# Kernel optimization log

Hardware: AMD Instinct MI355X
Metric: run time of the kernel (lower is better)

Reference implementation:

```python
import jax, jax.numpy as jnp
import numpy as np

EPS = 1e-5

def setup_inputs() -> dict:
    key = jax.random.key(0)
    k1, k2, k3 = jax.random.split(key, 3)
    B, C, V, L, O = 16, 64, 20000, 9, 64
    x = jax.random.normal(k1, (B, C, V), dtype=jnp.float32)
    spiral_idx = jax.random.randint(k2, (V, L), 0, V, dtype=jnp.int32)
    W = jax.random.normal(k3, (O, C * L), dtype=jnp.float32) * 0.02
    b = jnp.zeros((O,), dtype=jnp.float32)
    gamma = jnp.ones((O,), dtype=jnp.float32)
    beta = jnp.zeros((O,), dtype=jnp.float32)
    return {"x": x, "spiral_idx": spiral_idx, "W": W, "b": b, "gamma": gamma, "beta": beta}

def reference(x, spiral_idx, W, b, gamma, beta):
    B, C, V = x.shape
    L = spiral_idx.shape[1]
    # spiral neighbor gather: neigh[b,c,v,l] = x[b,c,spiral_idx[v,l]]  -> [B,C,V,L]
    neigh = x[:, :, spiral_idx]
    # faithful row-major reshape as in the torch module (mixes V and L)
    neigh = neigh.reshape(B, C * L, V)
    # 1x1 Conv1d == matmul over channel dim
    out = jnp.einsum('om,bmv->bov', W, neigh) + b[None, :, None]
    # BatchNorm1d (training mode: biased batch stats over B and V)
    mean = out.mean(axis=(0, 2), keepdims=True)
    var = ((out - mean) ** 2).mean(axis=(0, 2), keepdims=True)
    y = gamma[None, :, None] * (out - mean) * jax.lax.rsqrt(var + EPS) + beta[None, :, None]
    return jnp.maximum(y, 0.0)
```

## Files before the change

### kernel.cpp

```cpp
#include <hip/hip_runtime.h>
#include <hip/hip_bf16.h>
#include <cstdint>
#include <cstddef>

#define B_ 16
#define C_ 64
#define V_ 20000
#define L_ 9
#define O_ 64
#define K_ 576
#define NBV (B_*V_)
#define TPB 79
#define NB1 (TPB*8)
#define NBLK (TPB*16)

typedef short bf16x8 __attribute__((ext_vector_type(8)));
typedef float f32x4  __attribute__((ext_vector_type(4)));

__device__ inline unsigned short f2bf(float f) {
    union { float f; unsigned u; } x; x.f = f;
    unsigned r = (x.u + 0x7fffu + ((x.u >> 16) & 1u)) >> 16;
    return (unsigned short)r;
}

__global__ __launch_bounds__(256) void k_tx(const float* __restrict__ x,
                                            ushort* __restrict__ xTb) {
    __shared__ float t[C_][33];
    const int b  = blockIdx.y;
    const int v0 = blockIdx.x * 32;
    const int tid = threadIdx.x;
    {
        const int c  = tid >> 2;
        const int jj = tid & 3;
        const float* src = x + ((size_t)b * C_ + c) * V_ + v0 + jj * 8;
        float4 f0 = ((const float4*)src)[0];
        float4 f1 = ((const float4*)src)[1];
        t[c][jj*8+0] = f0.x; t[c][jj*8+1] = f0.y; t[c][jj*8+2] = f0.z; t[c][jj*8+3] = f0.w;
        t[c][jj*8+4] = f1.x; t[c][jj*8+5] = f1.y; t[c][jj*8+6] = f1.z; t[c][jj*8+7] = f1.w;
    }
    __syncthreads();
    {
        const int vl = tid & 31;
        const int cg = tid >> 5;
        union { ushort u[8]; uint4 v4; } pk;
#pragma unroll
        for (int i = 0; i < 8; ++i) pk.u[i] = f2bf(t[cg*8 + i][vl]);
        *(uint4*)(xTb + ((size_t)(b * V_ + v0 + vl)) * 64 + cg * 8) = pk.v4;
    }
}

__global__ __launch_bounds__(256) void k_tw(const float* __restrict__ W,
                                            ushort* __restrict__ Wtb) {
    int gid = blockIdx.x * 256 + threadIdx.x;
    if (gid >= O_ * K_) return;
    int o = gid / K_, kp = gid % K_;
    int tt = kp >> 6, c = kp & 63;
    Wtb[gid] = f2bf(W[o * K_ + c * L_ + tt]);
}

template<bool BF16Y>
__global__ __launch_bounds__(512, 4) void k_conv(const ushort* __restrict__ xTb,
                                                 const int*    __restrict__ S,
                                                 const ushort* __restrict__ Wtb,
                                                 const float*  __restrict__ bias,
                                                 float*  __restrict__ out,
                                                 ushort* __restrict__ yb,
                                                 float* __restrict__ ps,
                                                 float* __restrict__ pq) {
    __shared__ char lds[77824];
    char*  wlds = lds;
    float* sA   = (float*)(lds + 73728);
    float* sQ   = (float*)(lds + 75776);

    const int bid  = blockIdx.x;
    const int half = bid >= NB1;
    const int rbid = half ? bid - NB1 : bid;
    const int b    = (rbid & 7) | (half << 3);
    const int vt   = rbid >> 3;
    const int v0   = vt * 256;

    const int tid = threadIdx.x;
    const int w = tid >> 6;
    const int l = tid & 63;
    const int q = l >> 4;
    const int r = l & 15;

#pragma unroll
    for (int j = 0; j < 9; ++j) {
        const int id = tid + j * 512;
        const int u  = id >> 8;
        const int o  = (id >> 2) & 63;
        const int qq = id & 3;
        uint4 val = *(const uint4*)(Wtb + (size_t)o * K_ + u * 32 + qq * 8);
        *(uint4*)(wlds + u * 4096 + o * 64 + qq * 16) = val;
    }

    const int row0 = v0 + w * 32 + r;
    const int row1 = row0 + 16;
    const int r0c = row0 < V_ ? row0 : V_ - 1;
    const int r1c = row1 < V_ ? row1 : V_ - 1;
    int g0[L_], g1[L_];
#pragma unroll
    for (int t = 0; t < L_; ++t) { g0[t] = S[t * V_ + r0c]; g1[t] = S[t * V_ + r1c]; }

    const char* xb = (const char*)xTb + (size_t)b * V_ * 128 + q * 16;

    __syncthreads();

    f32x4 acc[2][4];
#pragma unroll
    for (int nt = 0; nt < 2; ++nt)
#pragma unroll
        for (int ot = 0; ot < 4; ++ot) acc[nt][ot] = (f32x4){0.f, 0.f, 0.f, 0.f};

    bf16x8 a0b[4], a1b[4];
#pragma unroll
    for (int u = 0; u < 4; ++u) {
        a0b[u] = *(const bf16x8*)(xb + (size_t)g0[u >> 1] * 128 + (u & 1) * 64);
        a1b[u] = *(const bf16x8*)(xb + (size_t)g1[u >> 1] * 128 + (u & 1) * 64);
    }

#pragma unroll
    for (int u = 0; u < 18; ++u) {
        const bf16x8 a0 = a0b[u & 3];
        const bf16x8 a1 = a1b[u & 3];
        const char* wu = wlds + u * 4096 + r * 64 + q * 16;
#pragma unroll
        for (int ot = 0; ot < 4; ++ot) {
            bf16x8 bo = *(const bf16x8*)(wu + ot * 1024);
            acc[0][ot] = __builtin_amdgcn_mfma_f32_16x16x32_bf16(a0, bo, acc[0][ot], 0, 0, 0);
            acc[1][ot] = __builtin_amdgcn_mfma_f32_16x16x32_bf16(a1, bo, acc[1][ot], 0, 0, 0);
        }
        if (u + 4 < 18) {
            const int un = u + 4;
            a0b[u & 3] = *(const bf16x8*)(xb + (size_t)g0[un >> 1] * 128 + (un & 1) * 64);
            a1b[u & 3] = *(const bf16x8*)(xb + (size_t)g1[un >> 1] * 128 + (un & 1) * 64);
        }
    }

    float ssum[4] = {0.f, 0.f, 0.f, 0.f};
    float qsum[4] = {0.f, 0.f, 0.f, 0.f};
#pragma unroll
    for (int ot = 0; ot < 4; ++ot) {
        const int o = ot * 16 + r;
        const float bo = bias[o];
#pragma unroll
        for (int nt = 0; nt < 2; ++nt) {
            const int v = v0 + w * 32 + nt * 16 + q * 4;
            if (v < V_) {
                float4 y;
                y.x = acc[nt][ot][0] + bo;
                y.y = acc[nt][ot][1] + bo;
                y.z = acc[nt][ot][2] + bo;
                y.w = acc[nt][ot][3] + bo;
                if (BF16Y) {
                    ushort4 u4;
                    u4.x = f2bf(y.x); u4.y = f2bf(y.y); u4.z = f2bf(y.z); u4.w = f2bf(y.w);
                    *(ushort4*)(yb + ((size_t)(b * O_ + o)) * V_ + v) = u4;
                } else {
                    *(float4*)(out + ((size_t)(b * O_ + o)) * V_ + v) = y;
                }
                ssum[ot] += y.x + y.y + y.z + y.w;
                qsum[ot] += y.x*y.x + y.y*y.y + y.z*y.z + y.w*y.w;
            }
        }
    }
#pragma unroll
    for (int ot = 0; ot < 4; ++ot) {
        float s  = ssum[ot], qq = qsum[ot];
        s  += __shfl_xor(s, 16);  s  += __shfl_xor(s, 32);
        qq += __shfl_xor(qq, 16); qq += __shfl_xor(qq, 32);
        if (l < 16) { sA[(ot*16 + l) * 8 + w] = s; sQ[(ot*16 + l) * 8 + w] = qq; }
    }
    __syncthreads();
    if (tid < 64) {
        float s = 0.f, qq = 0.f;
#pragma unroll
        for (int j = 0; j < 8; ++j) { s += sA[tid*8 + j]; qq += sQ[tid*8 + j]; }
        ps[bid * 64 + tid] = s;
        pq[bid * 64 + tid] = qq;
    }
}

__global__ __launch_bounds__(256) void k_fin(const float* __restrict__ ps,
                                             const float* __restrict__ pq,
                                             const float* __restrict__ gamma,
                                             const float* __restrict__ beta,
                                             float* __restrict__ ss) {
    __shared__ float as_[4], aq_[4];
    const int o = blockIdx.x, tid = threadIdx.x;
    float s = 0.f, q = 0.f;
    for (int i = tid; i < NBLK; i += 256) { s += ps[i*64 + o]; q += pq[i*64 + o]; }
#pragma unroll
    for (int off = 1; off < 64; off <<= 1) { s += __shfl_xor(s, off); q += __shfl_xor(q, off); }
    if ((tid & 63) == 0) { as_[tid >> 6] = s; aq_[tid >> 6] = q; }
    __syncthreads();
    if (tid == 0) {
        float S4 = as_[0] + as_[1] + as_[2] + as_[3];
        float Q4 = aq_[0] + aq_[1] + aq_[2] + aq_[3];
        const float n = 1.f / (float)NBV;
        float mean = S4 * n;
        float var  = fmaxf(Q4 * n - mean * mean, 0.f);
        float sc   = gamma[o] * rsqrtf(var + 1e-5f);
        ss[o]      = sc;
        ss[O_ + o] = beta[o] - mean * sc;
    }
}

__global__ __launch_bounds__(256) void k_norm_bf(const ushort* __restrict__ yb,
                                                 float* __restrict__ out,
                                                 const float* __restrict__ ss) {
    const int stride = gridDim.x * blockDim.x;
    const int total8 = (B_ * O_ * V_) / 8;
    for (int i = blockIdx.x * blockDim.x + threadIdx.x; i < total8; i += stride) {
        uint4 raw = ((const uint4*)yb)[i];
        const int row = (i * 8) / V_;
        const int o   = row & 63;
        const float sc = ss[o], sh = ss[O_ + o];
        const uint u32[4] = {raw.x, raw.y, raw.z, raw.w};
        float4 o0, o1;
        float vals[8];
#pragma unroll
        for (int j = 0; j < 4; ++j) {
            union { uint u; float f; } lo, hi;
            lo.u = (u32[j] & 0xffffu) << 16;
            hi.u = (u32[j] & 0xffff0000u);
            vals[2*j]   = lo.f;
            vals[2*j+1] = hi.f;
        }
        o0.x = fmaxf(fmaf(vals[0], sc, sh), 0.f);
        o0.y = fmaxf(fmaf(vals[1], sc, sh), 0.f);
        o0.z = fmaxf(fmaf(vals[2], sc, sh), 0.f);
        o0.w = fmaxf(fmaf(vals[3], sc, sh), 0.f);
        o1.x = fmaxf(fmaf(vals[4], sc, sh), 0.f);
        o1.y = fmaxf(fmaf(vals[5], sc, sh), 0.f);
        o1.z = fmaxf(fmaf(vals[6], sc, sh), 0.f);
        o1.w = fmaxf(fmaf(vals[7], sc, sh), 0.f);
        ((float4*)out)[2*i]   = o0;
        ((float4*)out)[2*i+1] = o1;
    }
}

__global__ __launch_bounds__(256) void k_norm_f32(float* __restrict__ out,
                                                  const float* __restrict__ ss) {
    const int stride = gridDim.x * blockDim.x;
    const int total4 = (B_ * O_ * V_) / 4;
    for (int i = blockIdx.x * blockDim.x + threadIdx.x; i < total4; i += stride) {
        float4 v4 = ((const float4*)out)[i];
        const int row = (i * 4) / V_;
        const int o   = row & 63;
        const float sc = ss[o], sh = ss[O_ + o];
        v4.x = fmaxf(fmaf(v4.x, sc, sh), 0.f);
        v4.y = fmaxf(fmaf(v4.y, sc, sh), 0.f);
        v4.z = fmaxf(fmaf(v4.z, sc, sh), 0.f);
        v4.w = fmaxf(fmaf(v4.w, sc, sh), 0.f);
        ((float4*)out)[i] = v4;
    }
}

extern "C" void kernel_launch(void* const* d_in, const int* in_sizes, int n_in,
                              void* d_out, int out_size, void* d_ws, size_t ws_size,
                              hipStream_t stream) {
    const float* x     = (const float*)d_in[0];
    const int*   S     = (const int*)  d_in[1];
    const float* W     = (const float*)d_in[2];
    const float* bias  = (const float*)d_in[3];
    const float* gamma = (const float*)d_in[4];
    const float* beta  = (const float*)d_in[5];
    float* out = (float*)d_out;

    char* ws = (char*)d_ws;
    const size_t xT_b = 40960000;
    const size_t wt_b = 73728;
    const size_t yb_b = 40960000;
    const size_t ps_b = (size_t)NBLK * 64 * 4;

    ushort* xTb = (ushort*)(ws);
    ushort* Wtb = (ushort*)(ws + xT_b);
    const bool bf16y = ws_size >= xT_b + wt_b + yb_b + 2 * ps_b + 512;

    ushort* yb; float* ps; float* pq; float* ssb;
    if (bf16y) {
        yb  = (ushort*)(ws + xT_b + wt_b);
        ps  = (float*) (ws + xT_b + wt_b + yb_b);
        pq  = (float*) (ws + xT_b + wt_b + yb_b + ps_b);
        ssb = (float*) (ws + xT_b + wt_b + yb_b + 2 * ps_b);
    } else {
        yb  = nullptr;
        ps  = (float*) (ws + xT_b + wt_b);
        pq  = (float*) (ws + xT_b + wt_b + ps_b);
        ssb = (float*) (ws + xT_b + wt_b + 2 * ps_b);
    }

    k_tw<<<dim3((O_ * K_ + 255) / 256), dim3(256), 0, stream>>>(W, Wtb);
    k_tx<<<dim3(625, 16),               dim3(256), 0, stream>>>(x, xTb);
    if (bf16y) {
        k_conv<true ><<<dim3(NBLK), dim3(512), 0, stream>>>(xTb, S, Wtb, bias, out, yb, ps, pq);
        k_fin<<<dim3(64), dim3(256), 0, stream>>>(ps, pq, gamma, beta, ssb);
        k_norm_bf<<<dim3(2048), dim3(256), 0, stream>>>(yb, out, ssb);
    } else {
        k_conv<false><<<dim3(NBLK), dim3(512), 0, stream>>>(xTb, S, Wtb, bias, out, yb, ps, pq);
        k_fin<<<dim3(64), dim3(256), 0, stream>>>(ps, pq, gamma, beta, ssb);
        k_norm_f32<<<dim3(2048), dim3(256), 0, stream>>>(out, ssb);
    }
}
```

Measured before the change: 115.5 us.

## Stream weights through small swizzled LDS chunks with smaller conv blocks

The conv kernel drops from 512 threads over 256 vertices to 256 threads over 128 vertices. It no longer stages the full 72KB weight matrix in LDS up front. Instead it streams weights in three 24KB chunks, loading each chunk into registers while the gathered activation loads are in flight, and uses an XOR swizzle to avoid LDS bank conflicts. The much smaller LDS footprint should let more blocks run per CU and overlap weight staging with the gathers. The cost is extra barriers per chunk, more blocks that each reload the weights, and a doubled count of partial-stat rows for the finalize kernel to sum.

New measurement: 118.2 us. 1.02x slower.

```diff
diff --git a/kernel.cpp b/kernel.cpp
--- a/kernel.cpp
+++ b/kernel.cpp
@@ -10,8 +10,7 @@
 #define O_ 64
 #define K_ 576
 #define NBV (B_*V_)
-#define TPB 79
-#define NB1 (TPB*8)
+#define TPB 157
 #define NBLK (TPB*16)
 
 typedef short bf16x8 __attribute__((ext_vector_type(8)));
@@ -22,6 +21,12 @@
     unsigned r = (x.u + 0x7fffu + ((x.u >> 16) & 1u)) >> 16;
     return (unsigned short)r;
 }
+
+#define BARRIER() do { \
+    asm volatile("s_waitcnt lgkmcnt(0)" ::: "memory"); \
+    __builtin_amdgcn_s_barrier(); \
+} while (0)
+#define VMW(N) asm volatile("s_waitcnt vmcnt(" #N ")" ::: "memory")
 
 __global__ __launch_bounds__(256) void k_tx(const float* __restrict__ x,
                                             ushort* __restrict__ xTb) {
@@ -59,41 +64,34 @@
 }
 
 template<bool BF16Y>
-__global__ __launch_bounds__(512, 4) void k_conv(const ushort* __restrict__ xTb,
-                                                 const int*    __restrict__ S,
-                                                 const ushort* __restrict__ Wtb,
-                                                 const float*  __restrict__ bias,
-                                                 float*  __restrict__ out,
-                                                 ushort* __restrict__ yb,
-                                                 float* __restrict__ ps,
-                                                 float* __restrict__ pq) {
-    __shared__ char lds[77824];
-    char*  wlds = lds;
-    float* sA   = (float*)(lds + 73728);
-    float* sQ   = (float*)(lds + 75776);
+__global__ __launch_bounds__(256) void k_conv(const ushort* __restrict__ xTb,
+                                              const int*    __restrict__ S,
+                                              const ushort* __restrict__ Wtb,
+                                              const float*  __restrict__ bias,
+                                              float*  __restrict__ out,
+                                              ushort* __restrict__ yb,
+                                              float* __restrict__ ps,
+                                              float* __restrict__ pq) {
+    __shared__ char lds[26624];
+    float* sA = (float*)(lds + 24576);
+    float* sQ = (float*)(lds + 25600);
 
     const int bid  = blockIdx.x;
-    const int half = bid >= NB1;
-    const int rbid = half ? bid - NB1 : bid;
-    const int b    = (rbid & 7) | (half << 3);
-    const int vt   = rbid >> 3;
-    const int v0   = vt * 256;
+    const int half = (bid >= TPB * 8) ? 1 : 0;
+    const int rem  = bid - half * (TPB * 8);
+    const int b    = (rem & 7) | (half << 3);
+    const int vt   = rem >> 3;
+    const int v0   = vt * 128;
 
     const int tid = threadIdx.x;
+    const int wso  = tid >> 2;
+    const int wsl  = tid & 3;
+    const int swzo = (wso >> 1) & 3;
     const int w = tid >> 6;
     const int l = tid & 63;
     const int q = l >> 4;
     const int r = l & 15;
-
-#pragma unroll
-    for (int j = 0; j < 9; ++j) {
-        const int id = tid + j * 512;
-        const int u  = id >> 8;
-        const int o  = (id >> 2) & 63;
-        const int qq = id & 3;
-        uint4 val = *(const uint4*)(Wtb + (size_t)o * K_ + u * 32 + qq * 8);
-        *(uint4*)(wlds + u * 4096 + o * 64 + qq * 16) = val;
-    }
+    const int fswz = (r >> 1) & 3;
 
     const int row0 = v0 + w * 32 + r;
     const int row1 = row0 + 16;
@@ -104,8 +102,7 @@
     for (int t = 0; t < L_; ++t) { g0[t] = S[t * V_ + r0c]; g1[t] = S[t * V_ + r1c]; }
 
     const char* xb = (const char*)xTb + (size_t)b * V_ * 128 + q * 16;
-
-    __syncthreads();
+    const ushort* wsrc = Wtb + (size_t)wso * K_ + wsl * 8;
 
     f32x4 acc[2][4];
 #pragma unroll
@@ -113,28 +110,44 @@
 #pragma unroll
         for (int ot = 0; ot < 4; ++ot) acc[nt][ot] = (f32x4){0.f, 0.f, 0.f, 0.f};
 
-    bf16x8 a0b[4], a1b[4];
-#pragma unroll
-    for (int u = 0; u < 4; ++u) {
-        a0b[u] = *(const bf16x8*)(xb + (size_t)g0[u >> 1] * 128 + (u & 1) * 64);
-        a1b[u] = *(const bf16x8*)(xb + (size_t)g1[u >> 1] * 128 + (u & 1) * 64);
-    }
-
-#pragma unroll
-    for (int u = 0; u < 18; ++u) {
-        const bf16x8 a0 = a0b[u & 3];
-        const bf16x8 a1 = a1b[u & 3];
-        const char* wu = wlds + u * 4096 + r * 64 + q * 16;
-#pragma unroll
-        for (int ot = 0; ot < 4; ++ot) {
-            bf16x8 bo = *(const bf16x8*)(wu + ot * 1024);
-            acc[0][ot] = __builtin_amdgcn_mfma_f32_16x16x32_bf16(a0, bo, acc[0][ot], 0, 0, 0);
-            acc[1][ot] = __builtin_amdgcn_mfma_f32_16x16x32_bf16(a1, bo, acc[1][ot], 0, 0, 0);
+    bf16x8 a0r[3], a1r[3];
+    uint4 wst[6];
+
+#pragma unroll
+    for (int ch = 0; ch < 3; ++ch) {
+#pragma unroll
+        for (int ks = 0; ks < 6; ++ks)
+            wst[ks] = *(const uint4*)(wsrc + (ch * 6 + ks) * 32);
+#pragma unroll
+        for (int pp = 0; pp < 3; ++pp) {
+            const int gs = ch * 6 + pp;
+            a0r[pp] = *(const bf16x8*)(xb + (size_t)g0[gs >> 1] * 128 + (gs & 1) * 64);
+            a1r[pp] = *(const bf16x8*)(xb + (size_t)g1[gs >> 1] * 128 + (gs & 1) * 64);
         }
-        if (u + 4 < 18) {
-            const int un = u + 4;
-            a0b[u & 3] = *(const bf16x8*)(xb + (size_t)g0[un >> 1] * 128 + (un & 1) * 64);
-            a1b[u & 3] = *(const bf16x8*)(xb + (size_t)g1[un >> 1] * 128 + (un & 1) * 64);
+        if (ch > 0) BARRIER();
+        VMW(6);
+#pragma unroll
+        for (int ks = 0; ks < 6; ++ks)
+            *(uint4*)(lds + ks * 4096 + wso * 64 + ((wsl ^ swzo) << 4)) = wst[ks];
+        BARRIER();
+
+#pragma unroll
+        for (int i6 = 0; i6 < 6; ++i6) {
+            const int slot = i6 % 3;
+            bf16x8 a0 = a0r[slot];
+            bf16x8 a1 = a1r[slot];
+            if (i6 < 3) {
+                const int gs = ch * 6 + i6 + 3;
+                a0r[slot] = *(const bf16x8*)(xb + (size_t)g0[gs >> 1] * 128 + (gs & 1) * 64);
+                a1r[slot] = *(const bf16x8*)(xb + (size_t)g1[gs >> 1] * 128 + (gs & 1) * 64);
+            }
+            const char* wu = lds + i6 * 4096 + r * 64 + ((q ^ fswz) << 4);
+#pragma unroll
+            for (int ot = 0; ot < 4; ++ot) {
+                bf16x8 bo = *(const bf16x8*)(wu + ot * 1024);
+                acc[0][ot] = __builtin_amdgcn_mfma_f32_16x16x32_bf16(a0, bo, acc[0][ot], 0, 0, 0);
+                acc[1][ot] = __builtin_amdgcn_mfma_f32_16x16x32_bf16(a1, bo, acc[1][ot], 0, 0, 0);
+            }
         }
     }
 
@@ -154,9 +167,9 @@
                 y.z = acc[nt][ot][2] + bo;
                 y.w = acc[nt][ot][3] + bo;
                 if (BF16Y) {
-                    ushort4 u4;
-                    u4.x = f2bf(y.x); u4.y = f2bf(y.y); u4.z = f2bf(y.z); u4.w = f2bf(y.w);
-                    *(ushort4*)(yb + ((size_t)(b * O_ + o)) * V_ + v) = u4;
+                    ushort4 u;
+                    u.x = f2bf(y.x); u.y = f2bf(y.y); u.z = f2bf(y.z); u.w = f2bf(y.w);
+                    *(ushort4*)(yb + ((size_t)(b * O_ + o)) * V_ + v) = u;
                 } else {
                     *(float4*)(out + ((size_t)(b * O_ + o)) * V_ + v) = y;
                 }
@@ -165,18 +178,19 @@
             }
         }
     }
+    __syncthreads();
 #pragma unroll
     for (int ot = 0; ot < 4; ++ot) {
         float s  = ssum[ot], qq = qsum[ot];
         s  += __shfl_xor(s, 16);  s  += __shfl_xor(s, 32);
         qq += __shfl_xor(qq, 16); qq += __shfl_xor(qq, 32);
-        if (l < 16) { sA[(ot*16 + l) * 8 + w] = s; sQ[(ot*16 + l) * 8 + w] = qq; }
+        if (l < 16) { sA[(ot*16 + l) * 4 + w] = s; sQ[(ot*16 + l) * 4 + w] = qq; }
     }
     __syncthreads();
     if (tid < 64) {
         float s = 0.f, qq = 0.f;
 #pragma unroll
-        for (int j = 0; j < 8; ++j) { s += sA[tid*8 + j]; qq += sQ[tid*8 + j]; }
+        for (int j = 0; j < 4; ++j) { s += sA[tid*4 + j]; qq += sQ[tid*4 + j]; }
         ps[bid * 64 + tid] = s;
         pq[bid * 64 + tid] = qq;
     }
@@ -295,11 +309,11 @@
     k_tw<<<dim3((O_ * K_ + 255) / 256), dim3(256), 0, stream>>>(W, Wtb);
     k_tx<<<dim3(625, 16),               dim3(256), 0, stream>>>(x, xTb);
     if (bf16y) {
-        k_conv<true ><<<dim3(NBLK), dim3(512), 0, stream>>>(xTb, S, Wtb, bias, out, yb, ps, pq);
+        k_conv<true ><<<dim3(NBLK), dim3(256), 0, stream>>>(xTb, S, Wtb, bias, out, yb, ps, pq);
         k_fin<<<dim3(64), dim3(256), 0, stream>>>(ps, pq, gamma, beta, ssb);
         k_norm_bf<<<dim3(2048), dim3(256), 0, stream>>>(yb, out, ssb);
     } else {
-        k_conv<false><<<dim3(NBLK), dim3(512), 0, stream>>>(xTb, S, Wtb, bias, out, yb, ps, pq);
+        k_conv<false><<<dim3(NBLK), dim3(256), 0, stream>>>(xTb, S, Wtb, bias, out, yb, ps, pq);
         k_fin<<<dim3(64), dim3(256), 0, stream>>>(ps, pq, gamma, beta, ssb);
         k_norm_f32<<<dim3(2048), dim3(256), 0, stream>>>(out, ssb);
     }
```
